# Kernel optimization log

Hardware: AMD Instinct MI355X
Metric: run time of the kernel (lower is better)

The kernel has to match this reference:

```python
import jax, jax.numpy as jnp
import numpy as np

N = 40962      # icosahedral mesh nodes
E = 245760     # ~degree-6 mesh edges
HD = 256       # hidden_dim
H = 8          # heads
C = HD // H    # out_ch per head = 32
EDIM = 16      # raw edge feature dim
L = 4          # num_layers


def setup_inputs() -> dict:
    key = jax.random.key(0)
    ks = iter(jax.random.split(key, 48))
    def rn(shape, scale=0.05):
        return jax.random.normal(next(ks), shape, dtype=jnp.float32) * scale
    inp = {}
    inp['mesh_enc'] = jax.random.normal(next(ks), (N, HD), dtype=jnp.float32)
    inp['edge_index'] = jax.random.randint(next(ks), (2, E), 0, N)
    inp['edge_attr'] = jax.random.normal(next(ks), (E, EDIM), dtype=jnp.float32)
    # edge input projection
    inp['ep_W'] = rn((EDIM, HD)); inp['ep_b'] = jnp.zeros((HD,), jnp.float32)
    # GATv2 layer 0 (in_ch=HD) and layers 1..L-1 stacked (in_ch=C)
    inp['Wl0'] = rn((HD, H, C));  inp['Wr0'] = rn((HD, H, C))
    inp['Wl'] = rn((L - 1, C, H, C)); inp['Wr'] = rn((L - 1, C, H, C))
    inp['We0'] = rn((HD, H, C));  inp['We'] = rn((L - 1, HD, H, C))
    inp['att0'] = rn((H, C));     inp['att'] = rn((L - 1, H, C))
    inp['Wres0'] = rn((HD, C));   inp['Wres'] = rn((L - 1, C, C))
    inp['bn0'] = jnp.zeros((C,), jnp.float32); inp['bn'] = jnp.zeros((L - 1, C), jnp.float32)
    # edge-update MLP (upd_hidden_dim = hidden_dim * ffn_ratio = HD)
    inp['Wu1_0'] = rn((2 * C + HD, HD)); inp['Wu1'] = rn((L - 1, 2 * C + HD, HD))
    inp['bu1_0'] = jnp.zeros((HD,), jnp.float32); inp['bu1'] = jnp.zeros((L - 1, HD), jnp.float32)
    inp['Wu2_0'] = rn((HD, HD)); inp['Wu2'] = rn((L - 1, HD, HD))
    inp['bu2_0'] = jnp.zeros((HD,), jnp.float32); inp['bu2'] = jnp.zeros((L - 1, HD), jnp.float32)
    # inter-layer LayerNorms (L-1 of them, over C)
    inp['ln_g'] = jnp.ones((L - 1, C), jnp.float32); inp['ln_b'] = jnp.zeros((L - 1, C), jnp.float32)
    # SGFormer-style global branch
    inp['Wq'] = rn((HD, H, C)); inp['Wk'] = rn((HD, H, C)); inp['Wv'] = rn((HD, H, C))
    inp['alpha_p'] = jnp.array(0.5, jnp.float32)
    inp['cn_g'] = jnp.ones((C,), jnp.float32); inp['cn_b'] = jnp.zeros((C,), jnp.float32)
    return inp


def _layernorm(x, g, b):
    mu = x.mean(-1, keepdims=True)
    var = x.var(-1, keepdims=True)
    return (x - mu) / jnp.sqrt(var + 1e-5) * g + b


def _segment_softmax(s, dst, n):
    smax = jax.ops.segment_max(s, dst, num_segments=n)
    smax = jnp.where(jnp.isfinite(smax), smax, 0.0)
    ex = jnp.exp(s - smax[dst])
    den = jax.ops.segment_sum(ex, dst, num_segments=n)
    return ex / (den[dst] + 1e-16)


def _gat(x, e, src, dst, Wl, Wr, We, att, Wres, bn, Wu1, bu1, Wu2, bu2):
    # GATv2 with edge features (PyG semantics), concat=False (head mean), residual
    xl = jnp.einsum('nd,dhc->nhc', x, Wl)          # [N,H,C]
    xr = jnp.einsum('nd,dhc->nhc', x, Wr)
    ee = jnp.einsum('ed,dhc->ehc', e, We)          # [E,H,C]
    m = xl[src] + xr[dst] + ee
    s = jnp.einsum('ehc,hc->eh', jax.nn.leaky_relu(m, 0.2), att)
    a = _segment_softmax(s, dst, x.shape[0])       # [E,H]
    agg = jax.ops.segment_sum(a[:, :, None] * xl[src], dst, num_segments=x.shape[0])
    out = agg.mean(axis=1) + x @ Wres + bn         # [N,C]
    # residual edge update MLP
    h = jnp.concatenate([out[src], out[dst], e], axis=-1)
    e_new = e + jax.nn.gelu(h @ Wu1 + bu1) @ Wu2 + bu2
    return out, e_new


def _sgformer(x, Wq, Wk, Wv):
    # SGFormer linear global attention, O(N)
    q = jnp.einsum('nd,dhc->nhc', x, Wq)
    k = jnp.einsum('nd,dhc->nhc', x, Wk)
    v = jnp.einsum('nd,dhc->nhc', x, Wv)
    qs = q / (jnp.linalg.norm(q, axis=-1, keepdims=True) + 1e-6)
    ks = k / (jnp.linalg.norm(k, axis=-1, keepdims=True) + 1e-6)
    n = jnp.float32(x.shape[0])
    kv = jnp.einsum('nhc,nhd->hcd', ks, v)
    num = jnp.einsum('nhc,hcd->nhd', qs, kv) + n * v
    den = jnp.einsum('nhc,hc->nh', qs, ks.sum(0)) + n
    return (num / den[..., None]).mean(axis=1)     # [N,C]


def reference(mesh_enc, edge_index, edge_attr, ep_W, ep_b, Wl0, Wr0, Wl, Wr, We0, We,
              att0, att, Wres0, Wres, bn0, bn, Wu1_0, Wu1, bu1_0, bu1, Wu2_0, Wu2,
              bu2_0, bu2, ln_g, ln_b, Wq, Wk, Wv, alpha_p, cn_g, cn_b):
    src, dst = edge_index[0], edge_index[1]
    e = edge_attr @ ep_W + ep_b
    x, e = _gat(mesh_enc, e, src, dst, Wl0, Wr0, We0, att0, Wres0, bn0,
                Wu1_0, bu1_0, Wu2_0, bu2_0)
    x = _layernorm(x, ln_g[0], ln_b[0])
    for i in range(L - 1):
        x, e = _gat(x, e, src, dst, Wl[i], Wr[i], We[i], att[i], Wres[i], bn[i],
                    Wu1[i], bu1[i], Wu2[i], bu2[i])
        if i < L - 2:
            x = _layernorm(x, ln_g[i + 1], ln_b[i + 1])
    trans_out = _sgformer(mesh_enc, Wq, Wk, Wv)
    alpha = jax.nn.sigmoid(alpha_p)
    return _layernorm(alpha * x + (1.0 - alpha) * trans_out, cn_g, cn_b)
```

## Files before the change

### kernel.cpp

```cpp
#include <hip/hip_runtime.h>
#include <hip/hip_bf16.h>
#include <math.h>

typedef __hip_bfloat16 bf16;
typedef __attribute__((ext_vector_type(8))) __bf16 bf16x8;
typedef __attribute__((ext_vector_type(4))) float f32x4;

#define NN 40962
#define NE 245760
#define HDIM 256
#define NH 8
#define CH 32

#define MT 64
#define KVB 512

__device__ __forceinline__ float b2f(bf16 v) { return __bfloat162float(v); }
__device__ __forceinline__ bf16 f2b(float v) { return __float2bfloat16(v); }
__device__ __forceinline__ unsigned short f2bs(float v) {
  bf16 b = __float2bfloat16(v);
  return __builtin_bit_cast(unsigned short, b);
}
__device__ __forceinline__ float bs2f(unsigned short u) {
  return __bfloat162float(__builtin_bit_cast(bf16, u));
}

__device__ __forceinline__ float fast_gelu(float x) {
  float x2 = x * x;
  float g = x * (0.7978845608028654f + 0.0356774081f * x2);
  float y = fminf(g * 2.885390081777927f, 60.f);
  float t = exp2f(y);
  float th = (t - 1.f) * __builtin_amdgcn_rcpf(t + 1.f);
  return 0.5f * x * (1.f + th);
}

__global__ __launch_bounds__(512) void k_edge_proj_mfma(
    const float* __restrict__ attr, const unsigned short* __restrict__ Weps,
    const float* __restrict__ bias, bf16* __restrict__ e) {
  __shared__ unsigned short At[MT][40];
  __shared__ unsigned short O[MT][264];
  int tid = threadIdx.x, l = tid & 63, w = tid >> 6;
  int lr = l & 15, lk = l >> 4;
  int base = blockIdx.x * MT;
  {
    int p = tid >> 3, q = tid & 7;
    if (q < 4) {
      float4 v = *reinterpret_cast<const float4*>(&attr[(size_t)(base + p) * 16 + q * 4]);
      unsigned short tmp[4] = {f2bs(v.x), f2bs(v.y), f2bs(v.z), f2bs(v.w)};
      *reinterpret_cast<uint2*>(&At[p][q * 4]) = *reinterpret_cast<const uint2*>(tmp);
    } else {
      unsigned short z[4] = {0, 0, 0, 0};
      *reinterpret_cast<uint2*>(&At[p][q * 4]) = *reinterpret_cast<const uint2*>(z);
    }
  }
  __syncthreads();

  int j0 = w * 32;
  f32x4 acc[4][2];
#pragma unroll
  for (int m = 0; m < 4; ++m)
#pragma unroll
    for (int n = 0; n < 2; ++n)
#pragma unroll
      for (int r = 0; r < 4; ++r) acc[m][n][r] = 0.f;
  {
    bf16x8 a[4], b[2];
#pragma unroll
    for (int m = 0; m < 4; ++m)
      a[m] = *reinterpret_cast<const bf16x8*>(&At[m * 16 + lr][lk * 8]);
#pragma unroll
    for (int n = 0; n < 2; ++n) {
      int nt = w * 2 + n;
      b[n] = *reinterpret_cast<const bf16x8*>(Weps + ((size_t)nt * 64 + l) * 8);
    }
#pragma unroll
    for (int m = 0; m < 4; ++m)
#pragma unroll
      for (int n = 0; n < 2; ++n)
        acc[m][n] = __builtin_amdgcn_mfma_f32_16x16x32_bf16(a[m], b[n], acc[m][n], 0, 0, 0);
  }
#pragma unroll
  for (int n = 0; n < 2; ++n) {
    int col = j0 + n * 16 + lr;
    float bv = bias[col];
#pragma unroll
    for (int m = 0; m < 4; ++m)
#pragma unroll
      for (int r = 0; r < 4; ++r)
        O[m * 16 + lk * 4 + r][col] = f2bs(acc[m][n][r] + bv);
  }
  __syncthreads();
  for (int t = tid; t < MT * 32; t += 512) {
    int p = t >> 5, c = t & 31;
    *reinterpret_cast<uint4*>(&e[(size_t)(base + p) * HDIM + c * 8]) =
        *reinterpret_cast<const uint4*>(&O[p][c * 8]);
  }
}

__global__ void k_csr_count(const int* __restrict__ dst, int* __restrict__ cnt) {
  int e = blockIdx.x * 256 + threadIdx.x;
  if (e < NE) atomicAdd(&cnt[dst[e]], 1);
}
__global__ void k_csr_scan(const int* __restrict__ cnt, int* __restrict__ rowptr,
                           int* __restrict__ cursor) {
  __shared__ int part[256];
  __shared__ int tot;
  int t = threadIdx.x;
  const int CHUNK = (NN + 255) / 256;
  int lo = t * CHUNK, hi = lo + CHUNK; if (hi > NN) hi = NN; if (lo > NN) lo = NN;
  int s = 0;
  for (int i = lo; i < hi; ++i) s += cnt[i];
  part[t] = s;
  __syncthreads();
  if (t == 0) {
    int run = 0;
    for (int i = 0; i < 256; ++i) { int v = part[i]; part[i] = run; run += v; }
    tot = run;
  }
  __syncthreads();
  int run = part[t];
  for (int i = lo; i < hi; ++i) { rowptr[i] = run; cursor[i] = run; run += cnt[i]; }
  if (t == 0) rowptr[NN] = tot;
}
__global__ void k_csr_fill(const int* __restrict__ src, const int* __restrict__ dst,
                           int* __restrict__ cursor, int2* __restrict__ csr) {
  int e = blockIdx.x * 256 + threadIdx.x;
  if (e >= NE) return;
  int p = atomicAdd(&cursor[dst[e]], 1);
  int2 v; v.x = e; v.y = src[e];
  csr[p] = v;
}

struct SwzP {
  const float *We0, *WeL, *Wl0, *Wr0, *Wq, *Wk, *Wv;
  const float *Wu1_0, *Wu1L, *Wu2_0, *Wu2L, *WlL, *WrL, *epW;
  unsigned short *wall, *w1s, *w2s, *w32s, *wep;
  int* cnt;
};
__device__ __forceinline__ void swz1(const float* __restrict__ W,
                                     unsigned short* __restrict__ out, int t, int Kdiv32) {
  int i = t & 7, l = (t >> 3) & 63;
  int k0 = (t >> 9) % Kdiv32;
  int n0 = t / (512 * Kdiv32);
  int k = k0 * 32 + (l >> 4) * 8 + i;
  int n = n0 * 16 + (l & 15);
  out[t] = f2bs(W[k * 256 + n]);
}
#define SWZ_NW (9 * 65536)
#define SWZ_N1 (3 * 81920)
#define SWZ_N2 (3 * 65536)
#define SWZ_N3 (6 * 8192)
#define SWZ_N4 8192
__global__ void k_swz_fused(SwzP P) {
  int gid = blockIdx.x * 256 + threadIdx.x;
  if (gid < SWZ_NW) {
    int mat = gid >> 16, t = gid & 65535;
    const float* W;
    switch (mat) {
      case 0: W = P.We0; break;
      case 1: W = P.WeL; break;
      case 2: W = P.WeL + 65536; break;
      case 3: W = P.WeL + 131072; break;
      case 4: W = P.Wl0; break;
      case 5: W = P.Wr0; break;
      case 6: W = P.Wq; break;
      case 7: W = P.Wk; break;
      default: W = P.Wv; break;
    }
    swz1(W, P.wall + (size_t)mat * 65536, t, 8);
  } else if (gid < SWZ_NW + SWZ_N1) {
    int idx = gid - SWZ_NW;
    int mat = idx / 81920, t = idx % 81920;
    const float* W = (mat == 0) ? P.Wu1_0 : P.Wu1L + (size_t)(mat - 1) * 81920;
    swz1(W, P.w1s + (size_t)mat * 81920, t, 10);
  } else if (gid < SWZ_NW + SWZ_N1 + SWZ_N2) {
    int idx = gid - SWZ_NW - SWZ_N1;
    int mat = idx >> 16, t = idx & 65535;
    const float* W = (mat == 0) ? P.Wu2_0 : P.Wu2L + (size_t)(mat - 1) * 65536;
    swz1(W, P.w2s + (size_t)mat * 65536, t, 8);
  } else if (gid < SWZ_NW + SWZ_N1 + SWZ_N2 + SWZ_N3) {
    int idx = gid - SWZ_NW - SWZ_N1 - SWZ_N2;
    int mat = idx >> 13, t = idx & 8191;
    int i = mat >> 1;
    const float* W = (mat & 1) ? P.WrL + (size_t)i * 8192 : P.WlL + (size_t)i * 8192;
    swz1(W, P.w32s + (size_t)mat * 8192, t, 1);
  } else if (gid < SWZ_NW + SWZ_N1 + SWZ_N2 + SWZ_N3 + SWZ_N4) {
    int t = gid - (SWZ_NW + SWZ_N1 + SWZ_N2 + SWZ_N3);
    int i = t & 7, l = (t >> 3) & 63;
    int n0 = t >> 9;
    int k = (l >> 4) * 8 + i;
    int n = n0 * 16 + (l & 15);
    P.wep[t] = (k < 16) ? f2bs(P.epW[k * 256 + n]) : (unsigned short)0;
  } else {
    int i = gid - (SWZ_NW + SWZ_N1 + SWZ_N2 + SWZ_N3 + SWZ_N4);
    if (i < NN) P.cnt[i] = 0;
  }
}

__global__ __launch_bounds__(512) void k_edge_score_mfma(
    const bf16* __restrict__ e, const unsigned short* __restrict__ Wes,
    const bf16* __restrict__ xl, const bf16* __restrict__ xr,
    const float* __restrict__ att, const int* __restrict__ src,
    const int* __restrict__ dst, float* __restrict__ sx) {
  __shared__ unsigned short Ae[MT][264];
  __shared__ float attS[HDIM];
  __shared__ int sidx[MT], didx[MT];
  int tid = threadIdx.x, l = tid & 63, w = tid >> 6;
  int lr = l & 15, lk = l >> 4;
  int base = blockIdx.x * MT;
  if (tid < HDIM) attS[tid] = att[tid];
  if (tid < MT) sidx[tid] = src[base + tid];
  else if (tid < 2 * MT) didx[tid - MT] = dst[base + tid - MT];
  for (int t = tid; t < MT * 32; t += 512) {
    int p = t >> 5, c = t & 31;
    *reinterpret_cast<uint4*>(&Ae[p][c * 8]) =
        *reinterpret_cast<const uint4*>(&e[(size_t)(base + p) * HDIM + c * 8]);
  }
  __syncthreads();

  f32x4 acc[4][2];
#pragma unroll
  for (int m = 0; m < 4; ++m)
#pragma unroll
    for (int n = 0; n < 2; ++n)
#pragma unroll
      for (int r = 0; r < 4; ++r) acc[m][n][r] = 0.f;
  for (int k0 = 0; k0 < 8; ++k0) {
    bf16x8 a[4], b[2];
#pragma unroll
    for (int m = 0; m < 4; ++m)
      a[m] = *reinterpret_cast<const bf16x8*>(&Ae[m * 16 + lr][k0 * 32 + lk * 8]);
#pragma unroll
    for (int n = 0; n < 2; ++n) {
      int nt = w * 2 + n;
      b[n] = *reinterpret_cast<const bf16x8*>(Wes + ((size_t)(nt * 8 + k0) * 64 + l) * 8);
    }
#pragma unroll
    for (int m = 0; m < 4; ++m)
#pragma unroll
      for (int n = 0; n < 2; ++n)
        acc[m][n] = __builtin_amdgcn_mfma_f32_16x16x32_bf16(a[m], b[n], acc[m][n], 0, 0, 0);
  }
  __syncthreads();

#pragma unroll
  for (int n = 0; n < 2; ++n) {
    int col = w * 32 + n * 16 + lr;
    float av = attS[col];
#pragma unroll
    for (int m = 0; m < 4; ++m)
#pragma unroll
      for (int r = 0; r < 4; ++r) {
        int row = m * 16 + lk * 4 + r;
        float xs = b2f(xl[(size_t)sidx[row] * HDIM + col]) +
                   b2f(xr[(size_t)didx[row] * HDIM + col]);
        float mm = acc[m][n][r] + xs;
        mm = (mm > 0.f) ? mm : 0.2f * mm;
        Ae[row][col] = f2bs(mm * av);
      }
  }
  __syncthreads();
  for (int pair = tid; pair < MT * NH; pair += 512) {
    int ed = pair >> 3, h = pair & 7;
    float s = 0.f;
#pragma unroll
    for (int c = 0; c < CH; ++c) s += bs2f(Ae[ed][h * CH + c]);
    sx[(size_t)(base + ed) * NH + h] = expf(s);
  }
}

template <int ID, bool LN>
__global__ __launch_bounds__(256) void k_gat_out(
    const int* __restrict__ rowptr, const int2* __restrict__ csr,
    const float* __restrict__ sx, const bf16* __restrict__ xl,
    const float* __restrict__ x, const float* __restrict__ Wres,
    const float* __restrict__ bn, const float* __restrict__ lng,
    const float* __restrict__ lnb, float* __restrict__ xpre,
    float* __restrict__ xpost) {
  int n = blockIdx.x;
  int j = threadIdx.x;
  int h = j >> 5, c = j & 31;
  int p0 = rowptr[n], p1 = rowptr[n + 1];
  float a = 0.f, dsum = 0.f;
  for (int p = p0; p < p1; ++p) {
    int2 es = csr[p];
    float ex = sx[(size_t)es.x * NH + h];
    a += ex * b2f(xl[(size_t)es.y * HDIM + j]);
    dsum += ex;
  }
  __shared__ float oh[HDIM];
  __shared__ float rs[NH][CH];
  __shared__ float oc[CH + 1];
  oh[j] = a / (dsum + 1e-16f);
  const int KS = ID / NH;
  float r = 0.f;
  for (int k = h * KS; k < (h + 1) * KS; ++k)
    r += x[(size_t)n * ID + k] * Wres[k * CH + c];
  rs[h][c] = r;
  __syncthreads();
  if (j < CH) {
    float o = 0.f;
#pragma unroll
    for (int hh = 0; hh < NH; ++hh) o += oh[hh * CH + j];
    o *= (1.f / NH);
    float rr = 0.f;
#pragma unroll
    for (int hh = 0; hh < NH; ++hh) rr += rs[hh][j];
    o += rr + bn[j];
    xpre[(size_t)n * CH + j] = o;
    oc[j] = o;
  }
  __syncthreads();
  if (LN && j < CH) {
    float mu = 0.f;
#pragma unroll
    for (int k = 0; k < CH; ++k) mu += oc[k];
    mu *= (1.f / CH);
    float var = 0.f;
#pragma unroll
    for (int k = 0; k < CH; ++k) { float d = oc[k] - mu; var += d * d; }
    var *= (1.f / CH);
    xpost[(size_t)n * CH + j] = (oc[j] - mu) * rsqrtf(var + 1e-5f) * lng[j] + lnb[j];
  }
}

__global__ __launch_bounds__(512) void k_edge_mlp_mfma(
    bf16* __restrict__ e, const float* __restrict__ xo,
    const int* __restrict__ src, const int* __restrict__ dst,
    const unsigned short* __restrict__ W1s, const float* __restrict__ bu1,
    const unsigned short* __restrict__ W2s, const float* __restrict__ bu2) {
  __shared__ unsigned short buf[MT][328];
  __shared__ int sidx[MT], didx[MT];
  int tid = threadIdx.x;
  int l = tid & 63;
  int w = tid >> 6;
  int base = blockIdx.x * MT;
  int lr = l & 15;
  int lk = l >> 4;

  if (tid < MT) sidx[tid] = src[base + tid];
  else if (tid < 2 * MT) didx[tid - MT] = dst[base + tid - MT];
  __syncthreads();

  for (int t = tid; t < MT * 32; t += 512) {
    int p = t >> 5, cc = t & 31;
    uint4 v = *reinterpret_cast<const uint4*>(&e[(size_t)(base + p) * HDIM + cc * 8]);
    *reinterpret_cast<uint4*>(&buf[p][64 + cc * 8]) = v;
  }
  for (int t = tid; t < MT * 64; t += 512) {
    int p = t >> 6, c = t & 63;
    float v = (c < CH) ? xo[(size_t)sidx[p] * CH + c]
                       : xo[(size_t)didx[p] * CH + (c - CH)];
    buf[p][c] = f2bs(v);
  }
  __syncthreads();

  int j0 = w * 32;

  f32x4 acc[4][2];
#pragma unroll
  for (int m = 0; m < 4; ++m)
#pragma unroll
    for (int n = 0; n < 2; ++n)
#pragma unroll
      for (int r = 0; r < 4; ++r) acc[m][n][r] = 0.f;

  for (int k0 = 0; k0 < 10; ++k0) {
    bf16x8 a[4], b[2];
#pragma unroll
    for (int m = 0; m < 4; ++m)
      a[m] = *reinterpret_cast<const bf16x8*>(&buf[m * 16 + lr][k0 * 32 + lk * 8]);
#pragma unroll
    for (int n = 0; n < 2; ++n) {
      int nt = w * 2 + n;
      b[n] = *reinterpret_cast<const bf16x8*>(W1s + ((size_t)(nt * 10 + k0) * 64 + l) * 8);
    }
#pragma unroll
    for (int m = 0; m < 4; ++m)
#pragma unroll
      for (int n = 0; n < 2; ++n)
        acc[m][n] = __builtin_amdgcn_mfma_f32_16x16x32_bf16(a[m], b[n], acc[m][n], 0, 0, 0);
  }
  __syncthreads();

#pragma unroll
  for (int n = 0; n < 2; ++n) {
    float bv = bu1[j0 + n * 16 + lr];
#pragma unroll
    for (int m = 0; m < 4; ++m)
#pragma unroll
      for (int r = 0; r < 4; ++r) {
        float g = fast_gelu(acc[m][n][r] + bv);
        buf[m * 16 + lk * 4 + r][j0 + n * 16 + lr] = f2bs(g);
      }
  }
  __syncthreads();

#pragma unroll
  for (int m = 0; m < 4; ++m)
#pragma unroll
    for (int n = 0; n < 2; ++n)
#pragma unroll
      for (int r = 0; r < 4; ++r) acc[m][n][r] = 0.f;

  for (int k0 = 0; k0 < 8; ++k0) {
    bf16x8 a[4], b[2];
#pragma unroll
    for (int m = 0; m < 4; ++m)
      a[m] = *reinterpret_cast<const bf16x8*>(&buf[m * 16 + lr][k0 * 32 + lk * 8]);
#pragma unroll
    for (int n = 0; n < 2; ++n) {
      int nt = w * 2 + n;
      b[n] = *reinterpret_cast<const bf16x8*>(W2s + ((size_t)(nt * 8 + k0) * 64 + l) * 8);
    }
#pragma unroll
    for (int m = 0; m < 4; ++m)
#pragma unroll
      for (int n = 0; n < 2; ++n)
        acc[m][n] = __builtin_amdgcn_mfma_f32_16x16x32_bf16(a[m], b[n], acc[m][n], 0, 0, 0);
  }
  __syncthreads();

#pragma unroll
  for (int n = 0; n < 2; ++n) {
    int col = j0 + n * 16 + lr;
    float bv = bu2[col];
#pragma unroll
    for (int m = 0; m < 4; ++m)
#pragma unroll
      for (int r = 0; r < 4; ++r)
        buf[m * 16 + lk * 4 + r][col] = f2bs(acc[m][n][r] + bv);
  }
  __syncthreads();

  for (int t = tid; t < MT * 32; t += 512) {
    int p = t >> 5, cc = t & 31;
    uint4 dv = *reinterpret_cast<const uint4*>(&buf[p][cc * 8]);
    uint4 ev = *reinterpret_cast<const uint4*>(&e[(size_t)(base + p) * HDIM + cc * 8]);
    const unsigned short* dd = (const unsigned short*)&dv;
    const unsigned short* ee = (const unsigned short*)&ev;
    unsigned short ov[8];
#pragma unroll
    for (int i = 0; i < 8; ++i) ov[i] = f2bs(bs2f(ee[i]) + bs2f(dd[i]));
    *reinterpret_cast<uint4*>(&e[(size_t)(base + p) * HDIM + cc * 8]) =
        *reinterpret_cast<const uint4*>(ov);
  }
}

__global__ __launch_bounds__(256) void k_node_proj0_mfma(
    const float* __restrict__ x, const unsigned short* __restrict__ Wls,
    const unsigned short* __restrict__ Wrs, bf16* __restrict__ xl,
    bf16* __restrict__ xr) {
  __shared__ unsigned short A[MT][264];
  __shared__ unsigned short O[MT][264];
  int tid = threadIdx.x, l = tid & 63, w = tid >> 6;
  int lr = l & 15, lk = l >> 4;
  int base = blockIdx.x * MT;
  for (int t = tid; t < MT * 64; t += 256) {
    int p = t >> 6, c = t & 63;
    int row = base + p; if (row >= NN) row = NN - 1;
    float4 v = *reinterpret_cast<const float4*>(&x[(size_t)row * HDIM + c * 4]);
    unsigned short tmp[4] = {f2bs(v.x), f2bs(v.y), f2bs(v.z), f2bs(v.w)};
    *reinterpret_cast<uint2*>(&A[p][c * 4]) = *reinterpret_cast<const uint2*>(tmp);
  }
  __syncthreads();
  int j0 = w * 64;
#pragma unroll
  for (int mtx = 0; mtx < 2; ++mtx) {
    const unsigned short* Ws = (mtx == 0) ? Wls : Wrs;
    bf16* outp = (mtx == 0) ? xl : xr;
    f32x4 acc[4][4];
#pragma unroll
    for (int m = 0; m < 4; ++m)
#pragma unroll
      for (int n = 0; n < 4; ++n)
#pragma unroll
        for (int r = 0; r < 4; ++r) acc[m][n][r] = 0.f;
    for (int k0 = 0; k0 < 8; ++k0) {
      bf16x8 a[4], b[4];
#pragma unroll
      for (int m = 0; m < 4; ++m)
        a[m] = *reinterpret_cast<const bf16x8*>(&A[m * 16 + lr][k0 * 32 + lk * 8]);
#pragma unroll
      for (int n = 0; n < 4; ++n) {
        int nt = (j0 >> 4) + n;
        b[n] = *reinterpret_cast<const bf16x8*>(Ws + ((size_t)(nt * 8 + k0) * 64 + l) * 8);
      }
#pragma unroll
      for (int m = 0; m < 4; ++m)
#pragma unroll
        for (int n = 0; n < 4; ++n)
          acc[m][n] = __builtin_amdgcn_mfma_f32_16x16x32_bf16(a[m], b[n], acc[m][n], 0, 0, 0);
    }
#pragma unroll
    for (int n = 0; n < 4; ++n)
#pragma unroll
      for (int m = 0; m < 4; ++m)
#pragma unroll
        for (int r = 0; r < 4; ++r)
          O[m * 16 + lk * 4 + r][j0 + n * 16 + lr] = f2bs(acc[m][n][r]);
    __syncthreads();
    for (int t = tid; t < MT * 32; t += 256) {
      int p = t >> 5, c = t & 31;
      if (base + p < NN)
        *reinterpret_cast<uint4*>(&outp[(size_t)(base + p) * HDIM + c * 8]) =
            *reinterpret_cast<const uint4*>(&O[p][c * 8]);
    }
    __syncthreads();
  }
}

__global__ __launch_bounds__(256) void k_node_projS_mfma(
    const float* __restrict__ x, const unsigned short* __restrict__ Wls,
    const unsigned short* __restrict__ Wrs, bf16* __restrict__ xl,
    bf16* __restrict__ xr) {
  __shared__ unsigned short A[MT][40];
  __shared__ unsigned short O[MT][264];
  int tid = threadIdx.x, l = tid & 63, w = tid >> 6;
  int lr = l & 15, lk = l >> 4;
  int base = blockIdx.x * MT;
  for (int t = tid; t < MT * 8; t += 256) {
    int p = t >> 3, q = t & 7;
    int row = base + p; if (row >= NN) row = NN - 1;
    float4 v = *reinterpret_cast<const float4*>(&x[(size_t)row * CH + q * 4]);
    unsigned short tmp[4] = {f2bs(v.x), f2bs(v.y), f2bs(v.z), f2bs(v.w)};
    *reinterpret_cast<uint2*>(&A[p][q * 4]) = *reinterpret_cast<const uint2*>(tmp);
  }
  __syncthreads();
  int j0 = w * 64;
#pragma unroll
  for (int mtx = 0; mtx < 2; ++mtx) {
    const unsigned short* Ws = (mtx == 0) ? Wls : Wrs;
    bf16* outp = (mtx == 0) ? xl : xr;
    f32x4 acc[4][4];
#pragma unroll
    for (int m = 0; m < 4; ++m)
#pragma unroll
      for (int n = 0; n < 4; ++n)
#pragma unroll
        for (int r = 0; r < 4; ++r) acc[m][n][r] = 0.f;
    bf16x8 a[4], b[4];
#pragma unroll
    for (int m = 0; m < 4; ++m)
      a[m] = *reinterpret_cast<const bf16x8*>(&A[m * 16 + lr][lk * 8]);
#pragma unroll
    for (int n = 0; n < 4; ++n) {
      int nt = (j0 >> 4) + n;
      b[n] = *reinterpret_cast<const bf16x8*>(Ws + ((size_t)nt * 64 + l) * 8);
    }
#pragma unroll
    for (int m = 0; m < 4; ++m)
#pragma unroll
      for (int n = 0; n < 4; ++n)
        acc[m][n] = __builtin_amdgcn_mfma_f32_16x16x32_bf16(a[m], b[n], acc[m][n], 0, 0, 0);
#pragma unroll
    for (int n = 0; n < 4; ++n)
#pragma unroll
      for (int m = 0; m < 4; ++m)
#pragma unroll
        for (int r = 0; r < 4; ++r)
          O[m * 16 + lk * 4 + r][j0 + n * 16 + lr] = f2bs(acc[m][n][r]);
    __syncthreads();
    for (int t = tid; t < MT * 32; t += 256) {
      int p = t >> 5, c = t & 31;
      if (base + p < NN)
        *reinterpret_cast<uint4*>(&outp[(size_t)(base + p) * HDIM + c * 8]) =
            *reinterpret_cast<const uint4*>(&O[p][c * 8]);
    }
    __syncthreads();
  }
}

__global__ __launch_bounds__(256) void k_sg_qkv_mfma(
    const float* __restrict__ x, const unsigned short* __restrict__ Wqs,
    const unsigned short* __restrict__ Wks, const unsigned short* __restrict__ Wvs,
    bf16* __restrict__ qs, bf16* __restrict__ ks, bf16* __restrict__ vv) {
  __shared__ unsigned short A[MT][264];
  __shared__ unsigned short O[MT][264];
  int tid = threadIdx.x, l = tid & 63, w = tid >> 6;
  int lr = l & 15, lk = l >> 4;
  int base = blockIdx.x * MT;
  for (int t = tid; t < MT * 64; t += 256) {
    int p = t >> 6, c = t & 63;
    int row = base + p; if (row >= NN) row = NN - 1;
    float4 v = *reinterpret_cast<const float4*>(&x[(size_t)row * HDIM + c * 4]);
    unsigned short tmp[4] = {f2bs(v.x), f2bs(v.y), f2bs(v.z), f2bs(v.w)};
    *reinterpret_cast<uint2*>(&A[p][c * 4]) = *reinterpret_cast<const uint2*>(tmp);
  }
  __syncthreads();
  int j0 = w * 64;
#pragma unroll
  for (int mtx = 0; mtx < 3; ++mtx) {
    const unsigned short* Ws = (mtx == 0) ? Wqs : (mtx == 1) ? Wks : Wvs;
    bf16* outp = (mtx == 0) ? qs : (mtx == 1) ? ks : vv;
    f32x4 acc[4][4];
#pragma unroll
    for (int m = 0; m < 4; ++m)
#pragma unroll
      for (int n = 0; n < 4; ++n)
#pragma unroll
        for (int r = 0; r < 4; ++r) acc[m][n][r] = 0.f;
    for (int k0 = 0; k0 < 8; ++k0) {
      bf16x8 a[4], b[4];
#pragma unroll
      for (int m = 0; m < 4; ++m)
        a[m] = *reinterpret_cast<const bf16x8*>(&A[m * 16 + lr][k0 * 32 + lk * 8]);
#pragma unroll
      for (int n = 0; n < 4; ++n) {
        int nt = (j0 >> 4) + n;
        b[n] = *reinterpret_cast<const bf16x8*>(Ws + ((size_t)(nt * 8 + k0) * 64 + l) * 8);
      }
#pragma unroll
      for (int m = 0; m < 4; ++m)
#pragma unroll
        for (int n = 0; n < 4; ++n)
          acc[m][n] = __builtin_amdgcn_mfma_f32_16x16x32_bf16(a[m], b[n], acc[m][n], 0, 0, 0);
    }
    if (mtx < 2) {
      float pa[4][4], pb[4][4];
#pragma unroll
      for (int m = 0; m < 4; ++m)
#pragma unroll
        for (int r = 0; r < 4; ++r) {
          pa[m][r] = acc[m][0][r] * acc[m][0][r] + acc[m][1][r] * acc[m][1][r];
          pb[m][r] = acc[m][2][r] * acc[m][2][r] + acc[m][3][r] * acc[m][3][r];
        }
#pragma unroll
      for (int off = 1; off < 16; off <<= 1) {
#pragma unroll
        for (int m = 0; m < 4; ++m)
#pragma unroll
          for (int r = 0; r < 4; ++r) {
            pa[m][r] += __shfl_xor(pa[m][r], off);
            pb[m][r] += __shfl_xor(pb[m][r], off);
          }
      }
#pragma unroll
      for (int m = 0; m < 4; ++m)
#pragma unroll
        for (int r = 0; r < 4; ++r) {
          float ra = 1.f / (sqrtf(pa[m][r]) + 1e-6f);
          float rb = 1.f / (sqrtf(pb[m][r]) + 1e-6f);
          acc[m][0][r] *= ra; acc[m][1][r] *= ra;
          acc[m][2][r] *= rb; acc[m][3][r] *= rb;
        }
    }
#pragma unroll
    for (int n = 0; n < 4; ++n)
#pragma unroll
      for (int m = 0; m < 4; ++m)
#pragma unroll
        for (int r = 0; r < 4; ++r)
          O[m * 16 + lk * 4 + r][j0 + n * 16 + lr] = f2bs(acc[m][n][r]);
    __syncthreads();
    for (int t = tid; t < MT * 32; t += 256) {
      int p = t >> 5, c = t & 31;
      if (base + p < NN)
        *reinterpret_cast<uint4*>(&outp[(size_t)(base + p) * HDIM + c * 8]) =
            *reinterpret_cast<const uint4*>(&O[p][c * 8]);
    }
    __syncthreads();
  }
}

__global__ void k_sg_kv1(const bf16* __restrict__ ks, const bf16* __restrict__ vv,
                         float* __restrict__ part) {
  int t = threadIdx.x;
  int h = t >> 5;
  float kvloc[CH];
  float ksl = 0.f;
#pragma unroll
  for (int d = 0; d < CH; ++d) kvloc[d] = 0.f;
  __shared__ float krow[HDIM], vrow[HDIM];
  for (int n = blockIdx.x; n < NN; n += KVB) {
    krow[t] = b2f(ks[(size_t)n * HDIM + t]);
    vrow[t] = b2f(vv[(size_t)n * HDIM + t]);
    __syncthreads();
    float kc = krow[t];
    ksl += kc;
#pragma unroll
    for (int d = 0; d < CH; ++d) kvloc[d] += kc * vrow[h * CH + d];
    __syncthreads();
  }
  float* dstp = part + (size_t)blockIdx.x * 8448;
#pragma unroll
  for (int d = 0; d < CH; d += 4)
    *reinterpret_cast<float4*>(&dstp[t * CH + d]) =
        *reinterpret_cast<const float4*>(&kvloc[d]);
  dstp[8192 + t] = ksl;
}

__global__ void k_sg_kv2(const float* __restrict__ part, float* __restrict__ kv,
                         float* __restrict__ ksum) {
  int idx = blockIdx.x * 256 + threadIdx.x;
  if (idx >= 8448) return;
  float s = 0.f;
  for (int b = 0; b < KVB; ++b) s += part[(size_t)b * 8448 + idx];
  if (idx < 8192) kv[idx] = s;
  else ksum[idx - 8192] = s;
}

__global__ void k_sg_final(const bf16* __restrict__ qs, const bf16* __restrict__ vv,
                           const float* __restrict__ kv, const float* __restrict__ ksum,
                           const float* __restrict__ xg, const float* __restrict__ alphap,
                           const float* __restrict__ cng, const float* __restrict__ cnb,
                           float* __restrict__ out) {
  int t = threadIdx.x;
  int d = t & 31, sub = t >> 5;
  __shared__ float qrow[8][HDIM];
  __shared__ float crow[8][CH];
  int n = blockIdx.x * 8 + sub;
  for (int tt = t; tt < 8 * HDIM; tt += 256) {
    int p = tt >> 8, k = tt & 255;
    int n2 = blockIdx.x * 8 + p;
    if (n2 < NN) qrow[p][k] = b2f(qs[(size_t)n2 * HDIM + k]);
  }
  __syncthreads();
  float alpha = 1.f / (1.f + expf(-alphap[0]));
  const float Nf = (float)NN;
  float comb = 0.f;
  if (n < NN) {
    float acc = 0.f;
#pragma unroll
    for (int h = 0; h < NH; ++h) {
      float nm = 0.f, dp = 0.f;
#pragma unroll 8
      for (int c = 0; c < CH; ++c) {
        float qv = qrow[sub][h * CH + c];
        nm += qv * kv[(h * CH + c) * CH + d];
        dp += qv * ksum[h * CH + c];
      }
      nm += Nf * b2f(vv[(size_t)n * HDIM + h * CH + d]);
      acc += nm / (dp + Nf);
    }
    float trans = acc * (1.f / NH);
    comb = alpha * xg[(size_t)n * CH + d] + (1.f - alpha) * trans;
    crow[sub][d] = comb;
  }
  __syncthreads();
  if (n < NN) {
    float mu = 0.f;
#pragma unroll
    for (int k = 0; k < CH; ++k) mu += crow[sub][k];
    mu *= (1.f / CH);
    float var = 0.f;
#pragma unroll
    for (int k = 0; k < CH; ++k) { float dv = crow[sub][k] - mu; var += dv * dv; }
    var *= (1.f / CH);
    float o = (comb - mu) * rsqrtf(var + 1e-5f) * cng[d] + cnb[d];
    out[(size_t)n * CH + d] = o;
  }
}

extern "C" void kernel_launch(void* const* d_in, const int* in_sizes, int n_in,
                              void* d_out, int out_size, void* d_ws, size_t ws_size,
                              hipStream_t stream) {
  const float* mesh  = (const float*)d_in[0];
  const int*   eidx  = (const int*)d_in[1];
  const float* eattr = (const float*)d_in[2];
  const float* epW   = (const float*)d_in[3];
  const float* epb   = (const float*)d_in[4];
  const float* Wl0   = (const float*)d_in[5];
  const float* Wr0   = (const float*)d_in[6];
  const float* WlL   = (const float*)d_in[7];
  const float* WrL   = (const float*)d_in[8];
  const float* We0   = (const float*)d_in[9];
  const float* WeL   = (const float*)d_in[10];
  const float* att0  = (const float*)d_in[11];
  const float* attL  = (const float*)d_in[12];
  const float* Wres0 = (const float*)d_in[13];
  const float* WresL = (const float*)d_in[14];
  const float* bn0   = (const float*)d_in[15];
  const float* bnL   = (const float*)d_in[16];
  const float* Wu1_0 = (const float*)d_in[17];
  const float* Wu1L  = (const float*)d_in[18];
  const float* bu1_0 = (const float*)d_in[19];
  const float* bu1L  = (const float*)d_in[20];
  const float* Wu2_0 = (const float*)d_in[21];
  const float* Wu2L  = (const float*)d_in[22];
  const float* bu2_0 = (const float*)d_in[23];
  const float* bu2L  = (const float*)d_in[24];
  const float* lng   = (const float*)d_in[25];
  const float* lnb   = (const float*)d_in[26];
  const float* Wq    = (const float*)d_in[27];
  const float* Wk    = (const float*)d_in[28];
  const float* Wv    = (const float*)d_in[29];
  const float* alphap= (const float*)d_in[30];
  const float* cng   = (const float*)d_in[31];
  const float* cnb   = (const float*)d_in[32];

  const int* src = eidx;
  const int* dst = eidx + NE;

  char* base = (char*)d_ws;
  size_t o = 0;
  auto alloc = [&](size_t bytes) -> char* {
    o = (o + 255) & ~(size_t)255;
    char* p = base + o;
    o += bytes;
    return p;
  };
  bf16* e    = (bf16*)alloc((size_t)NE * HDIM * 2);
  bf16* xl   = (bf16*)alloc((size_t)NN * HDIM * 2);
  bf16* xr   = (bf16*)alloc((size_t)NN * HDIM * 2);
  bf16* vvb  = (bf16*)alloc((size_t)NN * HDIM * 2);
  float* sbuf= (float*)alloc((size_t)NE * NH * 4);
  float* xa  = (float*)alloc((size_t)NN * CH * 4);
  float* xb  = (float*)alloc((size_t)NN * CH * 4);
  float* xc  = (float*)alloc((size_t)NN * CH * 4);
  float* kv  = (float*)alloc(NH * CH * CH * 4);
  float* ksum= (float*)alloc(NH * CH * 4);
  float* kvpart = (float*)alloc((size_t)KVB * 8448 * 4);
  unsigned short* w1s = (unsigned short*)alloc((size_t)3 * 320 * 256 * 2);
  unsigned short* w2s = (unsigned short*)alloc((size_t)3 * 256 * 256 * 2);
  unsigned short* wall= (unsigned short*)alloc((size_t)9 * 65536 * 2);
  unsigned short* w32s= (unsigned short*)alloc((size_t)6 * 32 * 256 * 2);
  unsigned short* wep = (unsigned short*)alloc((size_t)SWZ_N4 * 2);
  int* cnt    = (int*)alloc((size_t)NN * 4);
  int* rowptr = (int*)alloc((size_t)(NN + 1) * 4);
  int* cursor = (int*)alloc((size_t)NN * 4);
  int2* csr   = (int2*)alloc((size_t)NE * 8);
  if (ws_size < o) return;

  SwzP P;
  P.We0 = We0; P.WeL = WeL; P.Wl0 = Wl0; P.Wr0 = Wr0; P.Wq = Wq; P.Wk = Wk; P.Wv = Wv;
  P.Wu1_0 = Wu1_0; P.Wu1L = Wu1L; P.Wu2_0 = Wu2_0; P.Wu2L = Wu2L;
  P.WlL = WlL; P.WrL = WrL; P.epW = epW;
  P.wall = wall; P.w1s = w1s; P.w2s = w2s; P.w32s = w32s; P.wep = wep; P.cnt = cnt;
  int swz_total = SWZ_NW + SWZ_N1 + SWZ_N2 + SWZ_N3 + SWZ_N4 + NN;
  k_swz_fused<<<(swz_total + 255) / 256, 256, 0, stream>>>(P);

  k_csr_count<<<(NE + 255) / 256, 256, 0, stream>>>(dst, cnt);
  k_csr_scan<<<1, 256, 0, stream>>>(cnt, rowptr, cursor);
  k_csr_fill<<<(NE + 255) / 256, 256, 0, stream>>>(src, dst, cursor, csr);

  k_edge_proj_mfma<<<NE / MT, 512, 0, stream>>>(eattr, wep, epb, e);

  const float* xin = mesh;
  float* post = xb;
  for (int l = 0; l < 4; ++l) {
    const float *att_p, *Wres_p, *bn_p, *bu1_p, *bu2_p;
    if (l == 0) {
      att_p = att0; Wres_p = Wres0; bn_p = bn0; bu1_p = bu1_0; bu2_p = bu2_0;
    } else {
      int i = l - 1;
      att_p = attL + (size_t)i * HDIM;
      Wres_p = WresL + (size_t)i * CH * CH;
      bn_p = bnL + (size_t)i * CH;
      bu1_p = bu1L + (size_t)i * HDIM;
      bu2_p = bu2L + (size_t)i * HDIM;
    }

    if (l == 0)
      k_node_proj0_mfma<<<(NN + MT - 1) / MT, 256, 0, stream>>>(
          mesh, wall + (size_t)4 * 65536, wall + (size_t)5 * 65536, xl, xr);
    else
      k_node_projS_mfma<<<(NN + MT - 1) / MT, 256, 0, stream>>>(
          xin, w32s + (size_t)((l - 1) * 2 + 0) * 8192,
          w32s + (size_t)((l - 1) * 2 + 1) * 8192, xl, xr);

    k_edge_score_mfma<<<NE / MT, 512, 0, stream>>>(e, wall + (size_t)l * 65536,
                                                   xl, xr, att_p, src, dst, sbuf);

    if (l == 0)
      k_gat_out<HDIM, true><<<NN, 256, 0, stream>>>(rowptr, csr, sbuf, xl, xin, Wres_p,
                                                    bn_p, lng, lnb, xa, post);
    else if (l < 3)
      k_gat_out<CH, true><<<NN, 256, 0, stream>>>(rowptr, csr, sbuf, xl, xin, Wres_p,
                                                  bn_p, lng + (size_t)l * CH,
                                                  lnb + (size_t)l * CH, xa, post);
    else
      k_gat_out<CH, false><<<NN, 256, 0, stream>>>(rowptr, csr, sbuf, xl, xin, Wres_p,
                                                   bn_p, nullptr, nullptr, xa, nullptr);

    if (l < 3)
      k_edge_mlp_mfma<<<NE / MT, 512, 0, stream>>>(e, xa, src, dst,
                                                   w1s + (size_t)l * 320 * 256, bu1_p,
                                                   w2s + (size_t)l * 256 * 256, bu2_p);

    xin = post;
    post = (post == xb) ? xc : xb;
  }

  k_sg_qkv_mfma<<<(NN + MT - 1) / MT, 256, 0, stream>>>(
      mesh, wall + (size_t)6 * 65536, wall + (size_t)7 * 65536,
      wall + (size_t)8 * 65536, xl, xr, vvb);
  k_sg_kv1<<<KVB, 256, 0, stream>>>(xr, vvb, kvpart);
  k_sg_kv2<<<33, 256, 0, stream>>>(kvpart, kv, ksum);
  k_sg_final<<<(NN + 7) / 8, 256, 0, stream>>>(xl, vvb, kv, ksum, xa, alphap, cng, cnb,
                                               (float*)d_out);
}
```

Baseline: 1.492 ms.

## Scatter edge scores into CSR order and stage them in LDS for aggregation

The edge-score kernel now writes exp scores at each edge's CSR position through a pos array built in csr_fill, so the aggregation kernel reads scores contiguously instead of gathering by edge id. The aggregation kernel also stages chunks of source indices and scores in shared memory and unrolls the neighbor loop by four so several independent xl loads are in flight at once. This trades scattered writes in the score kernel, plus extra barriers per chunk, for coalesced reads and more memory parallelism in the gather.

```diff
diff --git a/kernel.cpp b/kernel.cpp
--- a/kernel.cpp
+++ b/kernel.cpp
@@ -123,12 +123,13 @@
   if (t == 0) rowptr[NN] = tot;
 }
 __global__ void k_csr_fill(const int* __restrict__ src, const int* __restrict__ dst,
-                           int* __restrict__ cursor, int2* __restrict__ csr) {
+                           int* __restrict__ cursor, int* __restrict__ csrsrc,
+                           int* __restrict__ pos) {
   int e = blockIdx.x * 256 + threadIdx.x;
   if (e >= NE) return;
   int p = atomicAdd(&cursor[dst[e]], 1);
-  int2 v; v.x = e; v.y = src[e];
-  csr[p] = v;
+  csrsrc[p] = src[e];
+  pos[e] = p;
 }
 
 struct SwzP {
@@ -201,7 +202,8 @@
     const bf16* __restrict__ e, const unsigned short* __restrict__ Wes,
     const bf16* __restrict__ xl, const bf16* __restrict__ xr,
     const float* __restrict__ att, const int* __restrict__ src,
-    const int* __restrict__ dst, float* __restrict__ sx) {
+    const int* __restrict__ dst, const int* __restrict__ pos,
+    float* __restrict__ sxc) {
   __shared__ unsigned short Ae[MT][264];
   __shared__ float attS[HDIM];
   __shared__ int sidx[MT], didx[MT];
@@ -265,14 +267,15 @@
     float s = 0.f;
 #pragma unroll
     for (int c = 0; c < CH; ++c) s += bs2f(Ae[ed][h * CH + c]);
-    sx[(size_t)(base + ed) * NH + h] = expf(s);
-  }
-}
-
+    sxc[(size_t)pos[base + ed] * NH + h] = expf(s);
+  }
+}
+
+#define GCHUNK 64
 template <int ID, bool LN>
 __global__ __launch_bounds__(256) void k_gat_out(
-    const int* __restrict__ rowptr, const int2* __restrict__ csr,
-    const float* __restrict__ sx, const bf16* __restrict__ xl,
+    const int* __restrict__ rowptr, const int* __restrict__ csrsrc,
+    const float* __restrict__ sxc, const bf16* __restrict__ xl,
     const float* __restrict__ x, const float* __restrict__ Wres,
     const float* __restrict__ bn, const float* __restrict__ lng,
     const float* __restrict__ lnb, float* __restrict__ xpre,
@@ -281,12 +284,31 @@
   int j = threadIdx.x;
   int h = j >> 5, c = j & 31;
   int p0 = rowptr[n], p1 = rowptr[n + 1];
+  __shared__ int srcS[GCHUNK];
+  __shared__ float exS[GCHUNK * NH];
   float a = 0.f, dsum = 0.f;
-  for (int p = p0; p < p1; ++p) {
-    int2 es = csr[p];
-    float ex = sx[(size_t)es.x * NH + h];
-    a += ex * b2f(xl[(size_t)es.y * HDIM + j]);
-    dsum += ex;
+  for (int pb = p0; pb < p1; pb += GCHUNK) {
+    int chunk = p1 - pb; if (chunk > GCHUNK) chunk = GCHUNK;
+    if (j < chunk) srcS[j] = csrsrc[pb + j];
+    for (int t = j; t < chunk * NH; t += 256) exS[t] = sxc[(size_t)pb * NH + t];
+    __syncthreads();
+    int i = 0;
+    for (; i + 4 <= chunk; i += 4) {
+      float e0 = exS[(i + 0) * NH + h], e1 = exS[(i + 1) * NH + h];
+      float e2 = exS[(i + 2) * NH + h], e3 = exS[(i + 3) * NH + h];
+      float x0 = b2f(xl[(size_t)srcS[i + 0] * HDIM + j]);
+      float x1 = b2f(xl[(size_t)srcS[i + 1] * HDIM + j]);
+      float x2 = b2f(xl[(size_t)srcS[i + 2] * HDIM + j]);
+      float x3 = b2f(xl[(size_t)srcS[i + 3] * HDIM + j]);
+      a += e0 * x0 + e1 * x1 + e2 * x2 + e3 * x3;
+      dsum += e0 + e1 + e2 + e3;
+    }
+    for (; i < chunk; ++i) {
+      float ev = exS[i * NH + h];
+      a += ev * b2f(xl[(size_t)srcS[i] * HDIM + j]);
+      dsum += ev;
+    }
+    __syncthreads();
   }
   __shared__ float oh[HDIM];
   __shared__ float rs[NH][CH];
@@ -804,7 +826,7 @@
   bf16* xl   = (bf16*)alloc((size_t)NN * HDIM * 2);
   bf16* xr   = (bf16*)alloc((size_t)NN * HDIM * 2);
   bf16* vvb  = (bf16*)alloc((size_t)NN * HDIM * 2);
-  float* sbuf= (float*)alloc((size_t)NE * NH * 4);
+  float* sxc = (float*)alloc((size_t)NE * NH * 4);
   float* xa  = (float*)alloc((size_t)NN * CH * 4);
   float* xb  = (float*)alloc((size_t)NN * CH * 4);
   float* xc  = (float*)alloc((size_t)NN * CH * 4);
@@ -819,7 +841,8 @@
   int* cnt    = (int*)alloc((size_t)NN * 4);
   int* rowptr = (int*)alloc((size_t)(NN + 1) * 4);
   int* cursor = (int*)alloc((size_t)NN * 4);
-  int2* csr   = (int2*)alloc((size_t)NE * 8);
+  int* csrsrc = (int*)alloc((size_t)NE * 4);
+  int* pos    = (int*)alloc((size_t)NE * 4);
   if (ws_size < o) return;
 
   SwzP P;
@@ -832,7 +855,7 @@
 
   k_csr_count<<<(NE + 255) / 256, 256, 0, stream>>>(dst, cnt);
   k_csr_scan<<<1, 256, 0, stream>>>(cnt, rowptr, cursor);
-  k_csr_fill<<<(NE + 255) / 256, 256, 0, stream>>>(src, dst, cursor, csr);
+  k_csr_fill<<<(NE + 255) / 256, 256, 0, stream>>>(src, dst, cursor, csrsrc, pos);
 
   k_edge_proj_mfma<<<NE / MT, 512, 0, stream>>>(eattr, wep, epb, e);
 
@@ -860,17 +883,17 @@
           w32s + (size_t)((l - 1) * 2 + 1) * 8192, xl, xr);
 
     k_edge_score_mfma<<<NE / MT, 512, 0, stream>>>(e, wall + (size_t)l * 65536,
-                                                   xl, xr, att_p, src, dst, sbuf);
+                                                   xl, xr, att_p, src, dst, pos, sxc);
 
     if (l == 0)
-      k_gat_out<HDIM, true><<<NN, 256, 0, stream>>>(rowptr, csr, sbuf, xl, xin, Wres_p,
+      k_gat_out<HDIM, true><<<NN, 256, 0, stream>>>(rowptr, csrsrc, sxc, xl, xin, Wres_p,
                                                     bn_p, lng, lnb, xa, post);
     else if (l < 3)
-      k_gat_out<CH, true><<<NN, 256, 0, stream>>>(rowptr, csr, sbuf, xl, xin, Wres_p,
+      k_gat_out<CH, true><<<NN, 256, 0, stream>>>(rowptr, csrsrc, sxc, xl, xin, Wres_p,
                                                   bn_p, lng + (size_t)l * CH,
                                                   lnb + (size_t)l * CH, xa, post);
     else
-      k_gat_out<CH, false><<<NN, 256, 0, stream>>>(rowptr, csr, sbuf, xl, xin, Wres_p,
+      k_gat_out<CH, false><<<NN, 256, 0, stream>>>(rowptr, csrsrc, sxc, xl, xin, Wres_p,
                                                    bn_p, nullptr, nullptr, xa, nullptr);
 
     if (l < 3)
```

Result: faster. 1.426 ms, median of 3 (-4.5%).
